# Performance work log

Measured on AMD Instinct MI355X. Metric: run time of the kernel, lower is better.

Reference implementation:

```python
import jax, jax.numpy as jnp
import numpy as np

NUM_USER = 100000
NUM_ITEM = 50000
N_NODES = NUM_USER + NUM_ITEM
N_EDGES = 4800000
DIM = 64
N_LAYERS = 4


def setup_inputs() -> dict:
    key = jax.random.key(0)
    k1, k2, k3, k4, k5 = jax.random.split(key, 5)
    user_emb = jax.random.normal(k1, (NUM_USER, DIM), dtype=jnp.float32)
    item_emb = jax.random.normal(k2, (NUM_ITEM, DIM), dtype=jnp.float32)
    edge_val = jax.random.uniform(k3, (N_EDGES,), dtype=jnp.float32)
    edge_row = jax.random.randint(k4, (N_EDGES,), 0, N_NODES, dtype=jnp.int32)
    edge_col = jax.random.randint(k5, (N_EDGES,), 0, N_NODES, dtype=jnp.int32)
    return {
        "user_emb": user_emb,
        "item_emb": item_emb,
        "edge_val": edge_val,
        "edge_row": edge_row,
        "edge_col": edge_col,
    }


def _spmm(edge_val, edge_row, edge_col, x):
    # out[r] = sum_{e: row[e]==r} val[e] * x[col[e]]  -- COO SpMM
    msgs = edge_val[:, None] * x[edge_col]  # [E, D]
    return jax.ops.segment_sum(msgs, edge_row, num_segments=N_NODES)


def reference(user_emb, item_emb, edge_val, edge_row, edge_col):
    # LightGCN.forward: concat embeddings, 4 spmm propagation layers,
    # return last layer split into user/item parts.
    x = jnp.concatenate([user_emb, item_emb], axis=0)  # [N, 64]
    for _ in range(N_LAYERS):
        x = _spmm(edge_val, edge_row, edge_col, x)
    return x[:NUM_USER], x[NUM_USER:]
```

## Files before the change

kernel.cpp:

```cpp
#include <hip/hip_runtime.h>

#define DIM 64
#define BSH 8
#define BROWS 256
#define MAXNB 1024
#define EPB 8192
#define BBT 1024

__global__ void zero_i(int* __restrict__ p, int n) {
    int i = blockIdx.x * blockDim.x + threadIdx.x;
    int stride = gridDim.x * blockDim.x;
    for (; i < n; i += stride) p[i] = 0;
}

__global__ void zero_f4(float* __restrict__ p, size_t n4) {
    size_t i = (size_t)blockIdx.x * blockDim.x + threadIdx.x;
    size_t stride = (size_t)gridDim.x * blockDim.x;
    float4 z = make_float4(0.f, 0.f, 0.f, 0.f);
    for (; i < n4; i += stride)
        reinterpret_cast<float4*>(p)[i] = z;
}

__device__ __forceinline__ unsigned int bf16_rne(float f) {
    unsigned int u = __float_as_uint(f);
    return (u + 0x7FFFu + ((u >> 16) & 1u)) >> 16;
}

__global__ void f32_to_bf16(const float* __restrict__ src,
                            unsigned short* __restrict__ dst, int n4) {
    int i = blockIdx.x * blockDim.x + threadIdx.x;
    int stride = gridDim.x * blockDim.x;
    for (; i < n4; i += stride) {
        float4 v = *reinterpret_cast<const float4*>(src + (size_t)i * 4);
        ushort4 o;
        o.x = (unsigned short)bf16_rne(v.x);
        o.y = (unsigned short)bf16_rne(v.y);
        o.z = (unsigned short)bf16_rne(v.z);
        o.w = (unsigned short)bf16_rne(v.w);
        *reinterpret_cast<ushort4*>(dst + (size_t)i * 4) = o;
    }
}

__global__ __launch_bounds__(BBT) void bucket_count(const int* __restrict__ row,
                                                    int* __restrict__ bcount,
                                                    int ne, int nb) {
    __shared__ int h[MAXNB];
    int t = threadIdx.x;
    for (int i = t; i < nb; i += BBT) h[i] = 0;
    __syncthreads();
    int base = blockIdx.x * EPB;
    int lim = base + EPB; if (lim > ne) lim = ne;
    for (int e = base + t; e < lim; e += BBT)
        atomicAdd(&h[row[e] >> BSH], 1);
    __syncthreads();
    for (int i = t; i < nb; i += BBT) {
        int c = h[i];
        if (c > 0) atomicAdd(&bcount[i], c);
    }
}

__global__ __launch_bounds__(1024) void scan_buckets(const int* __restrict__ bcount,
                                                     int* __restrict__ bstart,
                                                     int* __restrict__ bcursor, int nb) {
    __shared__ int s[1024];
    __shared__ int carry;
    int t = threadIdx.x;
    if (t == 0) carry = 0;
    __syncthreads();
    for (int off = 0; off < nb; off += 1024) {
        int i = off + t;
        int v = (i < nb) ? bcount[i] : 0;
        s[t] = v;
        __syncthreads();
        for (int d = 1; d < 1024; d <<= 1) {
            int a = (t >= d) ? s[t - d] : 0;
            __syncthreads();
            s[t] += a;
            __syncthreads();
        }
        int excl = carry + s[t] - v;
        if (i < nb) { bstart[i] = excl; bcursor[i] = excl; }
        __syncthreads();
        if (t == 1023) carry += s[1023];
        __syncthreads();
    }
    if (t == 0) bstart[nb] = carry;
}

__global__ __launch_bounds__(BBT) void bucket_scatter(const int* __restrict__ row,
                                                      const int* __restrict__ col,
                                                      const float* __restrict__ val,
                                                      int* __restrict__ bcursor,
                                                      int2* __restrict__ ebuf,
                                                      int ne, int nb) {
    __shared__ int h[MAXNB];
    int t = threadIdx.x;
    for (int i = t; i < nb; i += BBT) h[i] = 0;
    __syncthreads();
    int base = blockIdx.x * EPB;
    int lim = base + EPB; if (lim > ne) lim = ne;
    for (int e = base + t; e < lim; e += BBT)
        atomicAdd(&h[row[e] >> BSH], 1);
    __syncthreads();
    for (int i = t; i < nb; i += BBT) {
        int c = h[i];
        if (c > 0) h[i] = atomicAdd(&bcursor[i], c);
    }
    __syncthreads();
    for (int e = base + t; e < lim; e += BBT) {
        int r = row[e];
        int pos = atomicAdd(&h[r >> BSH], 1);
        ebuf[pos] = make_int2(col[e] | ((r & (BROWS - 1)) << 18), __float_as_int(val[e]));
    }
}

__global__ __launch_bounds__(512) void local_sort(const int2* __restrict__ ein,
                                                  const int* __restrict__ bstart,
                                                  int2* __restrict__ eout,
                                                  int* __restrict__ rowptr,
                                                  int nrows, int nb) {
    __shared__ int hist[BROWS];
    __shared__ int cur[BROWS];
    __shared__ int wsum[4];
    int b = blockIdx.x;
    int t = threadIdx.x;
    int beg = bstart[b], end = bstart[b + 1];
    if (t < BROWS) hist[t] = 0;
    __syncthreads();
    for (int e = beg + t; e < end; e += 512)
        atomicAdd(&hist[((unsigned)ein[e].x) >> 18], 1);
    __syncthreads();
    int v = 0, s = 0;
    if (t < BROWS) {
        v = hist[t];
        s = v;
        #pragma unroll
        for (int off = 1; off < 64; off <<= 1) {
            int a = __shfl_up(s, off);
            if ((t & 63) >= off) s += a;
        }
        if ((t & 63) == 63) wsum[t >> 6] = s;
    }
    __syncthreads();
    if (t < BROWS) {
        int woff = 0;
        #pragma unroll
        for (int w = 0; w < 4; ++w)
            if (w < (t >> 6)) woff += wsum[w];
        int excl = woff + s - v;
        cur[t] = excl;
        int r = (b << BSH) + t;
        if (r < nrows) rowptr[r] = beg + excl;
    }
    if (b == nb - 1 && t == 0) rowptr[nrows] = end;
    __syncthreads();
    for (int e = beg + t; e < end; e += 512) {
        int2 cv = ein[e];
        int rl = ((unsigned)cv.x) >> 18;
        int pos = beg + atomicAdd(&cur[rl], 1);
        eout[pos] = make_int2(cv.x & 0x3FFFF, cv.y);
    }
}

template<bool OUT16>
__global__ __launch_bounds__(256) void spmm_bf16(const int2* __restrict__ colval,
                                                 const int* __restrict__ rowptr,
                                                 const unsigned short* __restrict__ xb,
                                                 float* __restrict__ yf,
                                                 unsigned short* __restrict__ yb,
                                                 int nrows) {
    int wid  = (int)(((size_t)blockIdx.x * blockDim.x + threadIdx.x) >> 6);
    int lane = threadIdx.x & 63;
    if (wid >= nrows) return;
    int sub = lane >> 3;
    int q8  = (lane & 7) << 3;

    int beg = rowptr[wid];
    int end = rowptr[wid + 1];
    int len = end - beg;
    int nfull = len >> 3;

    float acc[8];
    #pragma unroll
    for (int k = 0; k < 8; ++k) acc[k] = 0.f;

    int e = beg + sub;
    #pragma unroll 4
    for (int g = 0; g < nfull; ++g, e += 8) {
        int2 cv = colval[e];
        float v = __int_as_float(cv.y);
        uint4 x = *reinterpret_cast<const uint4*>(xb + (size_t)cv.x * DIM + q8);
        acc[0] = fmaf(v, __uint_as_float(x.x << 16),          acc[0]);
        acc[1] = fmaf(v, __uint_as_float(x.x & 0xffff0000u),  acc[1]);
        acc[2] = fmaf(v, __uint_as_float(x.y << 16),          acc[2]);
        acc[3] = fmaf(v, __uint_as_float(x.y & 0xffff0000u),  acc[3]);
        acc[4] = fmaf(v, __uint_as_float(x.z << 16),          acc[4]);
        acc[5] = fmaf(v, __uint_as_float(x.z & 0xffff0000u),  acc[5]);
        acc[6] = fmaf(v, __uint_as_float(x.w << 16),          acc[6]);
        acc[7] = fmaf(v, __uint_as_float(x.w & 0xffff0000u),  acc[7]);
    }
    int rem = len & 7;
    if (sub < rem) {
        int2 cv = colval[e];
        float v = __int_as_float(cv.y);
        uint4 x = *reinterpret_cast<const uint4*>(xb + (size_t)cv.x * DIM + q8);
        acc[0] = fmaf(v, __uint_as_float(x.x << 16),          acc[0]);
        acc[1] = fmaf(v, __uint_as_float(x.x & 0xffff0000u),  acc[1]);
        acc[2] = fmaf(v, __uint_as_float(x.y << 16),          acc[2]);
        acc[3] = fmaf(v, __uint_as_float(x.y & 0xffff0000u),  acc[3]);
        acc[4] = fmaf(v, __uint_as_float(x.z << 16),          acc[4]);
        acc[5] = fmaf(v, __uint_as_float(x.z & 0xffff0000u),  acc[5]);
        acc[6] = fmaf(v, __uint_as_float(x.w << 16),          acc[6]);
        acc[7] = fmaf(v, __uint_as_float(x.w & 0xffff0000u),  acc[7]);
    }

    #pragma unroll
    for (int off = 8; off <= 32; off <<= 1) {
        #pragma unroll
        for (int k = 0; k < 8; ++k)
            acc[k] += __shfl_xor(acc[k], off);
    }

    if (sub == 0) {
        if (OUT16) {
            uint4 o;
            o.x = bf16_rne(acc[0]) | (bf16_rne(acc[1]) << 16);
            o.y = bf16_rne(acc[2]) | (bf16_rne(acc[3]) << 16);
            o.z = bf16_rne(acc[4]) | (bf16_rne(acc[5]) << 16);
            o.w = bf16_rne(acc[6]) | (bf16_rne(acc[7]) << 16);
            *reinterpret_cast<uint4*>(yb + (size_t)wid * DIM + q8) = o;
        } else {
            float* dst = yf + (size_t)wid * DIM + q8;
            *reinterpret_cast<float4*>(dst)     = make_float4(acc[0], acc[1], acc[2], acc[3]);
            *reinterpret_cast<float4*>(dst + 4) = make_float4(acc[4], acc[5], acc[6], acc[7]);
        }
    }
}

__global__ void spmm_atomic(const float* __restrict__ val,
                            const int* __restrict__ row,
                            const int* __restrict__ col,
                            const float* __restrict__ p0,
                            const float* __restrict__ p1,
                            int split,
                            float* __restrict__ y,
                            int nedges) {
    long long t = (long long)blockIdx.x * blockDim.x + threadIdx.x;
    int e = (int)(t >> 4);
    if (e >= nedges) return;
    int d = ((int)t & 15) << 2;
    float v = val[e];
    int r = row[e];
    int c = col[e];
    const float* src = (c < split) ? (p0 + (size_t)c * DIM)
                                   : (p1 + (size_t)(c - split) * DIM);
    float4 xv = *reinterpret_cast<const float4*>(src + d);
    float* o = y + (size_t)r * DIM + d;
    unsafeAtomicAdd(o + 0, v * xv.x);
    unsafeAtomicAdd(o + 1, v * xv.y);
    unsafeAtomicAdd(o + 2, v * xv.z);
    unsafeAtomicAdd(o + 3, v * xv.w);
}

extern "C" void kernel_launch(void* const* d_in, const int* in_sizes, int n_in,
                              void* d_out, int out_size, void* d_ws, size_t ws_size,
                              hipStream_t stream) {
    const float* user = (const float*)d_in[0];
    const float* item = (const float*)d_in[1];
    const float* val  = (const float*)d_in[2];
    const int*   row  = (const int*)d_in[3];
    const int*   col  = (const int*)d_in[4];

    int nU = in_sizes[0] / DIM;
    int nI = in_sizes[1] / DIM;
    int nE = in_sizes[2];
    int nN = nU + nI;
    int nb = (nN + BROWS - 1) >> BSH;
    size_t bufElems = (size_t)nN * DIM;
    size_t n4 = bufElems / 4;

    char* base = (char*)d_ws;
    size_t off = 0;
    auto alloc = [&](size_t bytes) -> void* {
        void* p = base + off;
        off = (off + bytes + 255) & ~(size_t)255;
        return p;
    };
    size_t xBytes = bufElems * sizeof(float);
    size_t eBytes = (size_t)nE * sizeof(int2);
    size_t bBytes = bufElems * 2 * sizeof(unsigned short);
    size_t r0 = xBytes > eBytes ? xBytes : eBytes;
    if (bBytes > r0) r0 = bBytes;
    char*  region0 = (char*)alloc(r0);
    int2*  colval  = (int2*)alloc(eBytes);
    int*   rowptr  = (int*)alloc((size_t)(nN + 1) * sizeof(int));
    int*   bcount  = (int*)alloc((size_t)nb * sizeof(int));
    int*   bstart  = (int*)alloc((size_t)(nb + 1) * sizeof(int));
    int*   bcursor = (int*)alloc((size_t)nb * sizeof(int));
    size_t needed  = off;

    float* Y = (float*)d_out;

    if (ws_size >= needed && nb <= MAXNB && nN < (1 << 18)) {
        int2* ebuf = (int2*)region0;
        unsigned short* B0 = (unsigned short*)region0;
        unsigned short* B1 = B0 + bufElems;

        int eb = (nE + EPB - 1) / EPB;
        zero_i<<<(nb + 255) / 256, 256, 0, stream>>>(bcount, nb);
        bucket_count<<<eb, BBT, 0, stream>>>(row, bcount, nE, nb);
        scan_buckets<<<1, 1024, 0, stream>>>(bcount, bstart, bcursor, nb);
        bucket_scatter<<<eb, BBT, 0, stream>>>(row, col, val, bcursor, ebuf, nE, nb);
        local_sort<<<nb, 512, 0, stream>>>(ebuf, bstart, colval, rowptr, nN, nb);

        int cu = (nU * DIM) / 4, ci = (nI * DIM) / 4;
        f32_to_bf16<<<2048, 256, 0, stream>>>(user, B0, cu);
        f32_to_bf16<<<2048, 256, 0, stream>>>(item, B0 + (size_t)nU * DIM, ci);

        int sgrid = (int)(((size_t)nN * 64 + 255) / 256);
        spmm_bf16<true ><<<sgrid, 256, 0, stream>>>(colval, rowptr, B0, nullptr, B1, nN);
        spmm_bf16<true ><<<sgrid, 256, 0, stream>>>(colval, rowptr, B1, nullptr, B0, nN);
        spmm_bf16<true ><<<sgrid, 256, 0, stream>>>(colval, rowptr, B0, nullptr, B1, nN);
        spmm_bf16<false><<<sgrid, 256, 0, stream>>>(colval, rowptr, B1, Y, nullptr, nN);
    } else {
        float* X = (float*)region0;
        int zblocks = (int)((n4 + 255) / 256);
        if (zblocks > 4096) zblocks = 4096;
        long long totalThreads = (long long)nE * 16;
        dim3 sgrid((unsigned)((totalThreads + 255) / 256));
        const float* Xu = X;
        const float* Xi = X + (size_t)nU * DIM;
        const float* Yu = Y;
        const float* Yi = Y + (size_t)nU * DIM;
        zero_f4<<<zblocks, 256, 0, stream>>>(X, n4);
        spmm_atomic<<<sgrid, 256, 0, stream>>>(val, row, col, user, item, nU, X, nE);
        zero_f4<<<zblocks, 256, 0, stream>>>(Y, n4);
        spmm_atomic<<<sgrid, 256, 0, stream>>>(val, row, col, Xu, Xi, nU, Y, nE);
        zero_f4<<<zblocks, 256, 0, stream>>>(X, n4);
        spmm_atomic<<<sgrid, 256, 0, stream>>>(val, row, col, Yu, Yi, nU, X, nE);
        zero_f4<<<zblocks, 256, 0, stream>>>(Y, n4);
        spmm_atomic<<<sgrid, 256, 0, stream>>>(val, row, col, Xu, Xi, nU, Y, nE);
    }
}
```

Measured before the change: 471.9 us.

## Replace global bucket scatter with per-chunk local sort and run-based merge

Replaces the count/scan/scatter/local_sort CSR build with three kernels. Each 8192-edge chunk is bucket-sorted locally into its own slice of the buffer and records per-bucket run offsets. A single-block scan then computes bucket starts, and a merge kernel per bucket gathers the runs from all chunks and row-sorts them into the CSR. This removes the global atomic cursor traffic and one full pass over the row array. In exchange there is a serial loop over roughly 586 chunks in the single-block scan and many short, scattered run reads in the merge.

Measured after the change: 570.8 us. +20.9%, slower.

```diff
diff --git a/kernel.cpp b/kernel.cpp
--- a/kernel.cpp
+++ b/kernel.cpp
@@ -3,15 +3,9 @@
 #define DIM 64
 #define BSH 8
 #define BROWS 256
-#define MAXNB 1024
+#define MAXNB 1023
 #define EPB 8192
-#define BBT 1024
-
-__global__ void zero_i(int* __restrict__ p, int n) {
-    int i = blockIdx.x * blockDim.x + threadIdx.x;
-    int stride = gridDim.x * blockDim.x;
-    for (; i < n; i += stride) p[i] = 0;
-}
+#define MAXNBLK 1024
 
 __global__ void zero_f4(float* __restrict__ p, size_t n4) {
     size_t i = (size_t)blockIdx.x * blockDim.x + threadIdx.x;
@@ -41,95 +35,104 @@
     }
 }
 
-__global__ __launch_bounds__(BBT) void bucket_count(const int* __restrict__ row,
-                                                    int* __restrict__ bcount,
-                                                    int ne, int nb) {
-    __shared__ int h[MAXNB];
+__global__ __launch_bounds__(1024) void chunk_sort(const int* __restrict__ row,
+                                                   const int* __restrict__ col,
+                                                   const float* __restrict__ val,
+                                                   int2* __restrict__ ebuf,
+                                                   int* __restrict__ runstart,
+                                                   int ne, int nb) {
+    __shared__ int h[1024];
+    __shared__ int sc[1024];
+    int blk = blockIdx.x;
     int t = threadIdx.x;
-    for (int i = t; i < nb; i += BBT) h[i] = 0;
-    __syncthreads();
-    int base = blockIdx.x * EPB;
+    int base = blk * EPB;
     int lim = base + EPB; if (lim > ne) lim = ne;
-    for (int e = base + t; e < lim; e += BBT)
+
+    h[t] = 0;
+    __syncthreads();
+    for (int e = base + t; e < lim; e += 1024)
         atomicAdd(&h[row[e] >> BSH], 1);
     __syncthreads();
-    for (int i = t; i < nb; i += BBT) {
-        int c = h[i];
-        if (c > 0) atomicAdd(&bcount[i], c);
-    }
-}
-
-__global__ __launch_bounds__(1024) void scan_buckets(const int* __restrict__ bcount,
-                                                     int* __restrict__ bstart,
-                                                     int* __restrict__ bcursor, int nb) {
-    __shared__ int s[1024];
-    __shared__ int carry;
-    int t = threadIdx.x;
-    if (t == 0) carry = 0;
-    __syncthreads();
-    for (int off = 0; off < nb; off += 1024) {
-        int i = off + t;
-        int v = (i < nb) ? bcount[i] : 0;
-        s[t] = v;
+
+    int v = h[t];
+    sc[t] = v;
+    __syncthreads();
+    for (int d = 1; d < 1024; d <<= 1) {
+        int a = (t >= d) ? sc[t - d] : 0;
         __syncthreads();
-        for (int d = 1; d < 1024; d <<= 1) {
-            int a = (t >= d) ? s[t - d] : 0;
-            __syncthreads();
-            s[t] += a;
-            __syncthreads();
-        }
-        int excl = carry + s[t] - v;
-        if (i < nb) { bstart[i] = excl; bcursor[i] = excl; }
+        sc[t] += a;
         __syncthreads();
-        if (t == 1023) carry += s[1023];
-        __syncthreads();
-    }
-    if (t == 0) bstart[nb] = carry;
-}
-
-__global__ __launch_bounds__(BBT) void bucket_scatter(const int* __restrict__ row,
-                                                      const int* __restrict__ col,
-                                                      const float* __restrict__ val,
-                                                      int* __restrict__ bcursor,
-                                                      int2* __restrict__ ebuf,
-                                                      int ne, int nb) {
-    __shared__ int h[MAXNB];
-    int t = threadIdx.x;
-    for (int i = t; i < nb; i += BBT) h[i] = 0;
-    __syncthreads();
-    int base = blockIdx.x * EPB;
-    int lim = base + EPB; if (lim > ne) lim = ne;
-    for (int e = base + t; e < lim; e += BBT)
-        atomicAdd(&h[row[e] >> BSH], 1);
-    __syncthreads();
-    for (int i = t; i < nb; i += BBT) {
-        int c = h[i];
-        if (c > 0) h[i] = atomicAdd(&bcursor[i], c);
-    }
-    __syncthreads();
-    for (int e = base + t; e < lim; e += BBT) {
+    }
+    int excl = sc[t] - v;
+    if (t <= nb)
+        runstart[(size_t)blk * (nb + 1) + t] = (t < nb) ? excl : (lim - base);
+    h[t] = excl;
+    __syncthreads();
+
+    for (int e = base + t; e < lim; e += 1024) {
         int r = row[e];
         int pos = atomicAdd(&h[r >> BSH], 1);
-        ebuf[pos] = make_int2(col[e] | ((r & (BROWS - 1)) << 18), __float_as_int(val[e]));
-    }
-}
-
-__global__ __launch_bounds__(512) void local_sort(const int2* __restrict__ ein,
-                                                  const int* __restrict__ bstart,
-                                                  int2* __restrict__ eout,
-                                                  int* __restrict__ rowptr,
-                                                  int nrows, int nb) {
+        ebuf[base + pos] = make_int2(col[e] | ((r & (BROWS - 1)) << 18),
+                                     __float_as_int(val[e]));
+    }
+}
+
+__global__ __launch_bounds__(1024) void bucket_scan(const int* __restrict__ runstart,
+                                                    int* __restrict__ bstart,
+                                                    int nb, int nblk) {
+    __shared__ int sc[1024];
+    int t = threadIdx.x;
+    int total = 0;
+    if (t < nb) {
+        for (int blk = 0; blk < nblk; ++blk) {
+            const int* rs = runstart + (size_t)blk * (nb + 1);
+            total += rs[t + 1] - rs[t];
+        }
+    }
+    sc[t] = total;
+    __syncthreads();
+    for (int d = 1; d < 1024; d <<= 1) {
+        int a = (t >= d) ? sc[t - d] : 0;
+        __syncthreads();
+        sc[t] += a;
+        __syncthreads();
+    }
+    if (t < nb) bstart[t] = sc[t] - total;
+    if (t == 0) bstart[nb] = sc[1023];
+}
+
+__global__ __launch_bounds__(1024) void merge_rowsort(const int2* __restrict__ ebuf,
+                                                      const int* __restrict__ runstart,
+                                                      const int* __restrict__ bstart,
+                                                      int2* __restrict__ colval,
+                                                      int* __restrict__ rowptr,
+                                                      int nrows, int nb, int nblk) {
+    __shared__ int runsrc[MAXNBLK];
+    __shared__ int runlen[MAXNBLK];
     __shared__ int hist[BROWS];
     __shared__ int cur[BROWS];
     __shared__ int wsum[4];
     int b = blockIdx.x;
     int t = threadIdx.x;
     int beg = bstart[b], end = bstart[b + 1];
+
+    for (int r = t; r < nblk; r += 1024) {
+        const int* rs = runstart + (size_t)r * (nb + 1) + b;
+        int s = rs[0], e2 = rs[1];
+        runsrc[r] = r * EPB + s;
+        runlen[r] = e2 - s;
+    }
     if (t < BROWS) hist[t] = 0;
     __syncthreads();
-    for (int e = beg + t; e < end; e += 512)
-        atomicAdd(&hist[((unsigned)ein[e].x) >> 18], 1);
-    __syncthreads();
+
+    int w = t >> 6, lane = t & 63;
+    for (int r = w; r < nblk; r += 16) {
+        int src = runsrc[r], len = runlen[r];
+        for (int i = lane; i < len; i += 64)
+            atomicAdd(&hist[((unsigned)ebuf[src + i].x) >> 18], 1);
+    }
+    __syncthreads();
+
     int v = 0, s = 0;
     if (t < BROWS) {
         v = hist[t];
@@ -145,20 +148,24 @@
     if (t < BROWS) {
         int woff = 0;
         #pragma unroll
-        for (int w = 0; w < 4; ++w)
-            if (w < (t >> 6)) woff += wsum[w];
+        for (int ww = 0; ww < 4; ++ww)
+            if (ww < (t >> 6)) woff += wsum[ww];
         int excl = woff + s - v;
         cur[t] = excl;
-        int r = (b << BSH) + t;
-        if (r < nrows) rowptr[r] = beg + excl;
+        int rr = (b << BSH) + t;
+        if (rr < nrows) rowptr[rr] = beg + excl;
     }
     if (b == nb - 1 && t == 0) rowptr[nrows] = end;
     __syncthreads();
-    for (int e = beg + t; e < end; e += 512) {
-        int2 cv = ein[e];
-        int rl = ((unsigned)cv.x) >> 18;
-        int pos = beg + atomicAdd(&cur[rl], 1);
-        eout[pos] = make_int2(cv.x & 0x3FFFF, cv.y);
+
+    for (int r = w; r < nblk; r += 16) {
+        int src = runsrc[r], len = runlen[r];
+        for (int i = lane; i < len; i += 64) {
+            int2 cv = ebuf[src + i];
+            int rl = ((unsigned)cv.x) >> 18;
+            int pos = atomicAdd(&cur[rl], 1);
+            colval[beg + pos] = make_int2(cv.x & 0x3FFFF, cv.y);
+        }
     }
 }
 
@@ -276,6 +283,7 @@
     int nE = in_sizes[2];
     int nN = nU + nI;
     int nb = (nN + BROWS - 1) >> BSH;
+    int nblk = (nE + EPB - 1) / EPB;
     size_t bufElems = (size_t)nN * DIM;
     size_t n4 = bufElems / 4;
 
@@ -287,31 +295,28 @@
         return p;
     };
     size_t xBytes = bufElems * sizeof(float);
-    size_t eBytes = (size_t)nE * sizeof(int2);
+    size_t eBytes = (size_t)nblk * EPB * sizeof(int2);
     size_t bBytes = bufElems * 2 * sizeof(unsigned short);
     size_t r0 = xBytes > eBytes ? xBytes : eBytes;
     if (bBytes > r0) r0 = bBytes;
-    char*  region0 = (char*)alloc(r0);
-    int2*  colval  = (int2*)alloc(eBytes);
-    int*   rowptr  = (int*)alloc((size_t)(nN + 1) * sizeof(int));
-    int*   bcount  = (int*)alloc((size_t)nb * sizeof(int));
-    int*   bstart  = (int*)alloc((size_t)(nb + 1) * sizeof(int));
-    int*   bcursor = (int*)alloc((size_t)nb * sizeof(int));
-    size_t needed  = off;
+    char*  region0  = (char*)alloc(r0);
+    int2*  colval   = (int2*)alloc((size_t)nE * sizeof(int2));
+    int*   rowptr   = (int*)alloc((size_t)(nN + 1) * sizeof(int));
+    int*   runstart = (int*)alloc((size_t)nblk * (nb + 1) * sizeof(int));
+    int*   bstart   = (int*)alloc((size_t)(nb + 1) * sizeof(int));
+    size_t needed   = off;
 
     float* Y = (float*)d_out;
 
-    if (ws_size >= needed && nb <= MAXNB && nN < (1 << 18)) {
+    if (ws_size >= needed && nb <= MAXNB && nblk <= MAXNBLK && nN < (1 << 18)) {
         int2* ebuf = (int2*)region0;
         unsigned short* B0 = (unsigned short*)region0;
         unsigned short* B1 = B0 + bufElems;
 
-        int eb = (nE + EPB - 1) / EPB;
-        zero_i<<<(nb + 255) / 256, 256, 0, stream>>>(bcount, nb);
-        bucket_count<<<eb, BBT, 0, stream>>>(row, bcount, nE, nb);
-        scan_buckets<<<1, 1024, 0, stream>>>(bcount, bstart, bcursor, nb);
-        bucket_scatter<<<eb, BBT, 0, stream>>>(row, col, val, bcursor, ebuf, nE, nb);
-        local_sort<<<nb, 512, 0, stream>>>(ebuf, bstart, colval, rowptr, nN, nb);
+        chunk_sort<<<nblk, 1024, 0, stream>>>(row, col, val, ebuf, runstart, nE, nb);
+        bucket_scan<<<1, 1024, 0, stream>>>(runstart, bstart, nb, nblk);
+        merge_rowsort<<<nb, 1024, 0, stream>>>(ebuf, runstart, bstart, colval, rowptr,
+                                               nN, nb, nblk);
 
         int cu = (nU * DIM) / 4, ci = (nI * DIM) / 4;
         f32_to_bf16<<<2048, 256, 0, stream>>>(user, B0, cu);
```

## Replace atomic bucket cursors with per-chunk count matrix and column scans

Applied to the files above, without the earlier changes.

The bucketing preprocessing now stores a per-chunk, per-bucket count matrix instead of accumulating counts into global atomics. A per-bucket scan across chunks then gives each chunk exact write offsets. This removes the zeroing kernel, the global atomics, and the histogram recount in the scatter kernel. It adds a count matrix in workspace (about 586 chunks by 586 buckets), an extra scan kernel with strided column reads, and limits on how many buckets and chunks are supported.

Result: faster. 459.1 us (-2.7%).

```diff
diff --git a/kernel.cpp b/kernel.cpp
--- a/kernel.cpp
+++ b/kernel.cpp
@@ -3,15 +3,9 @@
 #define DIM 64
 #define BSH 8
 #define BROWS 256
-#define MAXNB 1024
+#define MAXNB 1023
 #define EPB 8192
-#define BBT 1024
-
-__global__ void zero_i(int* __restrict__ p, int n) {
-    int i = blockIdx.x * blockDim.x + threadIdx.x;
-    int stride = gridDim.x * blockDim.x;
-    for (; i < n; i += stride) p[i] = 0;
-}
+#define MAXNBLK 1024
 
 __global__ void zero_f4(float* __restrict__ p, size_t n4) {
     size_t i = (size_t)blockIdx.x * blockDim.x + threadIdx.x;
@@ -41,75 +35,72 @@
     }
 }
 
-__global__ __launch_bounds__(BBT) void bucket_count(const int* __restrict__ row,
-                                                    int* __restrict__ bcount,
-                                                    int ne, int nb) {
-    __shared__ int h[MAXNB];
+__global__ __launch_bounds__(1024) void count_chunks(const int* __restrict__ row,
+                                                     int* __restrict__ runcnt,
+                                                     int ne, int nb) {
+    __shared__ int h[1024];
+    int blk = blockIdx.x, t = threadIdx.x;
+    h[t] = 0;
+    __syncthreads();
+    int base = blk * EPB;
+    int lim = base + EPB; if (lim > ne) lim = ne;
+    for (int e = base + t; e < lim; e += 1024)
+        atomicAdd(&h[row[e] >> BSH], 1);
+    __syncthreads();
+    if (t < nb) runcnt[(size_t)blk * nb + t] = h[t];
+}
+
+__global__ __launch_bounds__(1024) void scan_chunks(int* __restrict__ runcnt,
+                                                    int* __restrict__ btotal,
+                                                    int nb, int nblk) {
+    __shared__ int sc[1024];
+    int b = blockIdx.x, t = threadIdx.x;
+    int v = (t < nblk) ? runcnt[(size_t)t * nb + b] : 0;
+    sc[t] = v;
+    __syncthreads();
+    for (int d = 1; d < 1024; d <<= 1) {
+        int a = (t >= d) ? sc[t - d] : 0;
+        __syncthreads();
+        sc[t] += a;
+        __syncthreads();
+    }
+    if (t < nblk) runcnt[(size_t)t * nb + b] = sc[t] - v;
+    if (t == 1023) btotal[b] = sc[1023];
+}
+
+__global__ __launch_bounds__(1024) void scan_buckets(const int* __restrict__ btotal,
+                                                     int* __restrict__ bstart, int nb) {
+    __shared__ int sc[1024];
     int t = threadIdx.x;
-    for (int i = t; i < nb; i += BBT) h[i] = 0;
-    __syncthreads();
-    int base = blockIdx.x * EPB;
+    int v = (t < nb) ? btotal[t] : 0;
+    sc[t] = v;
+    __syncthreads();
+    for (int d = 1; d < 1024; d <<= 1) {
+        int a = (t >= d) ? sc[t - d] : 0;
+        __syncthreads();
+        sc[t] += a;
+        __syncthreads();
+    }
+    if (t < nb) bstart[t] = sc[t] - v;
+    if (t == 0) bstart[nb] = sc[1023];
+}
+
+__global__ __launch_bounds__(1024) void scatter2(const int* __restrict__ row,
+                                                 const int* __restrict__ col,
+                                                 const float* __restrict__ val,
+                                                 const int* __restrict__ bstart,
+                                                 const int* __restrict__ runcnt,
+                                                 int2* __restrict__ ebuf,
+                                                 int ne, int nb) {
+    __shared__ int cur[1024];
+    int blk = blockIdx.x, t = threadIdx.x;
+    if (t < nb) cur[t] = bstart[t] + runcnt[(size_t)blk * nb + t];
+    __syncthreads();
+    int base = blk * EPB;
     int lim = base + EPB; if (lim > ne) lim = ne;
-    for (int e = base + t; e < lim; e += BBT)
-        atomicAdd(&h[row[e] >> BSH], 1);
-    __syncthreads();
-    for (int i = t; i < nb; i += BBT) {
-        int c = h[i];
-        if (c > 0) atomicAdd(&bcount[i], c);
-    }
-}
-
-__global__ __launch_bounds__(1024) void scan_buckets(const int* __restrict__ bcount,
-                                                     int* __restrict__ bstart,
-                                                     int* __restrict__ bcursor, int nb) {
-    __shared__ int s[1024];
-    __shared__ int carry;
-    int t = threadIdx.x;
-    if (t == 0) carry = 0;
-    __syncthreads();
-    for (int off = 0; off < nb; off += 1024) {
-        int i = off + t;
-        int v = (i < nb) ? bcount[i] : 0;
-        s[t] = v;
-        __syncthreads();
-        for (int d = 1; d < 1024; d <<= 1) {
-            int a = (t >= d) ? s[t - d] : 0;
-            __syncthreads();
-            s[t] += a;
-            __syncthreads();
-        }
-        int excl = carry + s[t] - v;
-        if (i < nb) { bstart[i] = excl; bcursor[i] = excl; }
-        __syncthreads();
-        if (t == 1023) carry += s[1023];
-        __syncthreads();
-    }
-    if (t == 0) bstart[nb] = carry;
-}
-
-__global__ __launch_bounds__(BBT) void bucket_scatter(const int* __restrict__ row,
-                                                      const int* __restrict__ col,
-                                                      const float* __restrict__ val,
-                                                      int* __restrict__ bcursor,
-                                                      int2* __restrict__ ebuf,
-                                                      int ne, int nb) {
-    __shared__ int h[MAXNB];
-    int t = threadIdx.x;
-    for (int i = t; i < nb; i += BBT) h[i] = 0;
-    __syncthreads();
-    int base = blockIdx.x * EPB;
-    int lim = base + EPB; if (lim > ne) lim = ne;
-    for (int e = base + t; e < lim; e += BBT)
-        atomicAdd(&h[row[e] >> BSH], 1);
-    __syncthreads();
-    for (int i = t; i < nb; i += BBT) {
-        int c = h[i];
-        if (c > 0) h[i] = atomicAdd(&bcursor[i], c);
-    }
-    __syncthreads();
-    for (int e = base + t; e < lim; e += BBT) {
+    for (int e = base + t; e < lim; e += 1024) {
         int r = row[e];
-        int pos = atomicAdd(&h[r >> BSH], 1);
+        int pos = atomicAdd(&cur[r >> BSH], 1);
         ebuf[pos] = make_int2(col[e] | ((r & (BROWS - 1)) << 18), __float_as_int(val[e]));
     }
 }
@@ -276,6 +267,7 @@
     int nE = in_sizes[2];
     int nN = nU + nI;
     int nb = (nN + BROWS - 1) >> BSH;
+    int nblk = (nE + EPB - 1) / EPB;
     size_t bufElems = (size_t)nN * DIM;
     size_t n4 = bufElems / 4;
 
@@ -294,23 +286,22 @@
     char*  region0 = (char*)alloc(r0);
     int2*  colval  = (int2*)alloc(eBytes);
     int*   rowptr  = (int*)alloc((size_t)(nN + 1) * sizeof(int));
-    int*   bcount  = (int*)alloc((size_t)nb * sizeof(int));
+    int*   runcnt  = (int*)alloc((size_t)nblk * nb * sizeof(int));
+    int*   btotal  = (int*)alloc((size_t)nb * sizeof(int));
     int*   bstart  = (int*)alloc((size_t)(nb + 1) * sizeof(int));
-    int*   bcursor = (int*)alloc((size_t)nb * sizeof(int));
     size_t needed  = off;
 
     float* Y = (float*)d_out;
 
-    if (ws_size >= needed && nb <= MAXNB && nN < (1 << 18)) {
+    if (ws_size >= needed && nb <= MAXNB && nblk <= MAXNBLK && nN < (1 << 18)) {
         int2* ebuf = (int2*)region0;
         unsigned short* B0 = (unsigned short*)region0;
         unsigned short* B1 = B0 + bufElems;
 
-        int eb = (nE + EPB - 1) / EPB;
-        zero_i<<<(nb + 255) / 256, 256, 0, stream>>>(bcount, nb);
-        bucket_count<<<eb, BBT, 0, stream>>>(row, bcount, nE, nb);
-        scan_buckets<<<1, 1024, 0, stream>>>(bcount, bstart, bcursor, nb);
-        bucket_scatter<<<eb, BBT, 0, stream>>>(row, col, val, bcursor, ebuf, nE, nb);
+        count_chunks<<<nblk, 1024, 0, stream>>>(row, runcnt, nE, nb);
+        scan_chunks<<<nb, 1024, 0, stream>>>(runcnt, btotal, nb, nblk);
+        scan_buckets<<<1, 1024, 0, stream>>>(btotal, bstart, nb);
+        scatter2<<<nblk, 1024, 0, stream>>>(row, col, val, bstart, runcnt, ebuf, nE, nb);
         local_sort<<<nb, 512, 0, stream>>>(ebuf, bstart, colval, rowptr, nN, nb);
 
         int cu = (nU * DIM) / 4, ci = (nI * DIM) / 4;
```
